# Optimization experiments

Measured on AMD Instinct MI355X. Metric: run time of the kernel, lower is better.

## Reference

```python
import jax, jax.numpy as jnp
import numpy as np

N_NODES = 50000


def _scatter_softmax(alpha, row, n):
    # per-row-segment softmax over edges
    amax = jax.ops.segment_max(alpha, row, num_segments=n)
    amax = jnp.where(jnp.isfinite(amax), amax, 0.0)
    ex = jnp.exp(alpha - amax[row])
    den = jax.ops.segment_sum(ex, row, num_segments=n)
    return ex / den[row]


def setup_inputs() -> dict:
    key = jax.random.key(0)
    ks = jax.random.split(key, 10)
    N, E, H, NC, D = N_NODES, 500000, 128, 3, 3
    kv_in = H + NC * NC  # 137 (edges_in_d = 0)
    h = jax.random.normal(ks[0], (N, H), jnp.float32)
    coord = jax.random.normal(ks[1], (N, NC, D), jnp.float32)
    row = jax.random.randint(ks[2], (E,), 0, N, jnp.int32)
    col = jax.random.randint(ks[3], (E,), 0, N, jnp.int32)
    Wq = jax.random.normal(ks[4], (H, H), jnp.float32) / np.sqrt(H)
    bq = jnp.zeros((H,), jnp.float32)
    Wkv = jax.random.normal(ks[5], (kv_in, 2 * H), jnp.float32) / np.sqrt(kv_in)
    bkv = jnp.zeros((2 * H,), jnp.float32)
    Wc1 = jax.random.normal(ks[6], (H, 4 * H), jnp.float32) / np.sqrt(H)
    # torch.nn.init.xavier_uniform_(..., gain=0.001)
    Wc2 = jax.random.normal(ks[7], (4 * H, NC), jnp.float32) * 0.001
    return {"h": h, "coord": coord, "row": row, "col": col,
            "Wq": Wq, "bq": bq, "Wkv": Wkv, "bkv": bkv, "Wc1": Wc1, "Wc2": Wc2}


def reference(h, coord, row, col, Wq, bq, Wkv, bkv, Wc1, Wc2):
    N = h.shape[0]
    nc = coord.shape[1]
    # coord2radial (rm_F_norm=True: no normalization)
    coord_diff = coord[row] - coord[col]                      # [E, nc, d]
    radial = jnp.einsum('ecd,efd->ecf', coord_diff, coord_diff)  # [E, nc, nc]
    radial_flat = radial.reshape(radial.shape[0], nc * nc)
    # att_model: gather -> Q / KV linears -> interleaved k,v split
    q = h[row] @ Wq + bq                                      # [E, H]
    target_feat = jnp.concatenate([radial_flat, h[col]], axis=1)
    kv = target_feat @ Wkv + bkv                              # [E, 2H]
    k, v = kv[:, 0::2], kv[:, 1::2]
    alpha = jnp.sum(q * k, axis=1)                            # [E]
    alpha = _scatter_softmax(alpha, row, N)
    # node_model: scatter_sum aggregate (dropout is identity at eval)
    agg = jax.ops.segment_sum(alpha[:, None] * v, row, num_segments=N)
    h_out = h + agg
    # coord_model: coord_mlp(v) (MLPwoBias: linear -> SiLU -> linear, no biases)
    coord_v = alpha[:, None] * (jax.nn.silu(v @ Wc1) @ Wc2)   # [E, nc]
    trans = coord_diff * coord_v[:, :, None]                  # [E, nc, d]
    cagg = jax.ops.segment_sum(trans, row, num_segments=N)
    coord_out = coord + jnp.clip(cagg, -10.0, 10.0)
    return (h_out, coord_out, alpha)
```

## Files before the change

### kernel.cpp

```cpp
#include <hip/hip_runtime.h>

#define H 128
#define KV 256
#define CPAD 16

typedef short bf16x8 __attribute__((ext_vector_type(8)));
typedef float f32x4 __attribute__((ext_vector_type(4)));
union FragU { uint4 u; bf16x8 s; };

#define LOG2E 1.44269504088896f
#define LN2   0.69314718055995f

__device__ __forceinline__ float bf2f(unsigned short u) {
  return __uint_as_float(((unsigned)u) << 16);
}
__device__ __forceinline__ unsigned short f2bf(float f) {
  unsigned b = __float_as_uint(f);
  b += 0x7FFFu + ((b >> 16) & 1u);
  return (unsigned short)(b >> 16);
}
__device__ __forceinline__ float fsilu(float x) {
  return x * __builtin_amdgcn_rcpf(1.f + __expf(-x));
}
__device__ __forceinline__ float fexp2(float x) {
  float r;
  asm("v_exp_f32 %0, %1" : "=v"(r) : "v"(x));
  return r;
}
__device__ __forceinline__ float fsilu2(float y) {
  return y * __builtin_amdgcn_rcpf(1.f + fexp2(-y));
}
__device__ __forceinline__ void rad6_from_cd(const float cd[9], float r6[6]) {
  r6[0] = cd[0]*cd[0] + cd[1]*cd[1] + cd[2]*cd[2];
  r6[1] = cd[3]*cd[3] + cd[4]*cd[4] + cd[5]*cd[5];
  r6[2] = cd[6]*cd[6] + cd[7]*cd[7] + cd[8]*cd[8];
  r6[3] = cd[0]*cd[3] + cd[1]*cd[4] + cd[2]*cd[5];
  r6[4] = cd[0]*cd[6] + cd[1]*cd[7] + cd[2]*cd[8];
  r6[5] = cd[3]*cd[6] + cd[4]*cd[7] + cd[5]*cd[8];
}
__constant__ int c_pa[6] = {0,4,8,1,2,5};
__constant__ int c_pb[6] = {0,0,0,3,6,7};

__global__ __launch_bounds__(256) void k_zero(float* __restrict__ p, int n) {
  int i = blockIdx.x * 256 + threadIdx.x;
  if (i < n) p[i] = 0.f;
}
__global__ __launch_bounds__(256) void k_sentinel(float* __restrict__ out, int n) {
  int i = blockIdx.x * 256 + threadIdx.x;
  if (i < n) out[i] = 1000.0f;
}

__global__ __launch_bounds__(256) void k_prep_w1(const float* __restrict__ Wc1,
                                                 uint4* __restrict__ w1f) {
  int t = blockIdx.x*256 + threadIdx.x;
  int g = t >> 6, lane = t & 63;
  int q = g >> 5, kk = (g >> 3) & 3, mt = g & 7;
  int o = q*128 + mt*16 + (lane & 15);
  int kbase = kk*32 + (lane >> 4)*8;
  unsigned s[8];
  #pragma unroll
  for (int j = 0; j < 8; ++j) s[j] = f2bf(Wc1[(kbase+j)*512 + o] * LOG2E);
  uint4 u;
  u.x = s[0] | (s[1]<<16); u.y = s[2] | (s[3]<<16);
  u.z = s[4] | (s[5]<<16); u.w = s[6] | (s[7]<<16);
  w1f[g*64 + lane] = u;
}

__global__ __launch_bounds__(256) void k_prep_wcat(
    const float* __restrict__ Wq, const float* __restrict__ Wkv,
    uint4* __restrict__ wcat_hi, uint4* __restrict__ wcat_lo)
{
  int t = blockIdx.x*256 + threadIdx.x;
  if (t >= 96*64) return;
  int g = t >> 6, lane = t & 63;
  int mt = g & 7, kk = (g >> 3) & 3, q = g >> 5;
  int oo = mt*16 + (lane & 15);
  int kbase = kk*32 + (lane >> 4)*8;
  unsigned shi[8], slo[8];
  #pragma unroll
  for (int j = 0; j < 8; ++j) {
    int k = kbase + j;
    float w;
    if (q == 0)      w = Wq[k*H + oo];
    else if (q == 1) w = Wkv[(9 + k)*KV + 2*oo];
    else             w = Wkv[(9 + k)*KV + 2*oo + 1];
    unsigned hi = f2bf(w);
    float lo = w - bf2f((unsigned short)hi);
    shi[j] = hi; slo[j] = f2bf(lo);
  }
  uint4 uh, ul;
  uh.x = shi[0]|(shi[1]<<16); uh.y = shi[2]|(shi[3]<<16);
  uh.z = shi[4]|(shi[5]<<16); uh.w = shi[6]|(shi[7]<<16);
  ul.x = slo[0]|(slo[1]<<16); ul.y = slo[2]|(slo[3]<<16);
  ul.z = slo[4]|(slo[5]<<16); ul.w = slo[6]|(slo[7]<<16);
  wcat_hi[g*64 + lane] = uh;
  wcat_lo[g*64 + lane] = ul;
}

__global__ __launch_bounds__(256) void k_prep_wr6(const float* __restrict__ Wkv,
                                                  const float* __restrict__ Wc1,
                                                  float* __restrict__ Wr6) {
  int idx = blockIdx.x*256 + threadIdx.x;
  if (idx >= 6*512) return;
  int d = idx >> 9, o = idx & 511;
  float s = 0.f;
  for (int k = 0; k < 128; ++k) {
    float w = Wkv[c_pa[d]*KV + 2*k + 1];
    if (d >= 3) w += Wkv[c_pb[d]*KV + 2*k + 1];
    s += w * Wc1[k*512 + o];
  }
  Wr6[d*512 + o] = s;
}

__global__ __launch_bounds__(256) void k_prep_ar6(
    const float* __restrict__ Wr6, const float* __restrict__ Wc2,
    uint4* __restrict__ ar6f, float* __restrict__ w2p)
{
  int t = threadIdx.x;
  for (int i = t; i < 512; i += 256) {
    int ch = i;
    unsigned b0 = (unsigned)f2bf(Wr6[0*512+ch]*LOG2E) | ((unsigned)f2bf(Wr6[1*512+ch]*LOG2E)<<16);
    unsigned b1 = (unsigned)f2bf(Wr6[2*512+ch]*LOG2E) | ((unsigned)f2bf(Wr6[3*512+ch]*LOG2E)<<16);
    unsigned b2 = (unsigned)f2bf(Wr6[4*512+ch]*LOG2E) | ((unsigned)f2bf(Wr6[5*512+ch]*LOG2E)<<16);
    ar6f[i] = make_uint4(b0, b1, b2, 0u);
  }
  for (int i = t; i < 1536; i += 256) {
    int i4 = i & 3, rest = i >> 2;
    int k = rest % 3, g = rest / 3;
    int ch = (g >> 2)*16 + (g & 3)*4 + i4;
    w2p[i] = Wc2[ch*3 + k] * LN2;
  }
}

__global__ __launch_bounds__(256) void k_hist2(const int* __restrict__ row,
                                               const int* __restrict__ col,
                                               int* __restrict__ cr,
                                               int* __restrict__ cc, int E) {
  int e = blockIdx.x*256 + threadIdx.x;
  if (e >= E) return;
  atomicAdd(&cr[(size_t)row[e]*CPAD], 1);
  atomicAdd(&cc[(size_t)col[e]*CPAD], 1);
}

__global__ __launch_bounds__(1024) void k_scan2(
    const int* __restrict__ cr, int* __restrict__ rstart, int* __restrict__ rcur,
    const int* __restrict__ cc, int* __restrict__ cstart, int* __restrict__ ccur,
    int n) {
  const int* counts = (blockIdx.x == 0) ? cr : cc;
  int* start = (blockIdx.x == 0) ? rstart : cstart;
  int* cursor = (blockIdx.x == 0) ? rcur : ccur;
  __shared__ int wsum[16];
  __shared__ int carry_s;
  const int tid = threadIdx.x, lane = tid & 63, wid = tid >> 6;
  if (tid == 0) carry_s = 0;
  __syncthreads();
  for (int base = 0; base < n; base += 1024) {
    int i = base + tid;
    int v = (i < n) ? counts[(size_t)i*CPAD] : 0;
    int s = v;
    #pragma unroll
    for (int off = 1; off < 64; off <<= 1) {
      int t = __shfl_up(s, off, 64);
      if (lane >= off) s += t;
    }
    if (lane == 63) wsum[wid] = s;
    __syncthreads();
    if (wid == 0 && lane < 16) {
      int w = wsum[lane];
      #pragma unroll
      for (int off = 1; off < 16; off <<= 1) {
        int t = __shfl_up(w, off, 16);
        if (lane >= off) w += t;
      }
      wsum[lane] = w;
    }
    __syncthreads();
    int wexcl = (wid == 0) ? 0 : wsum[wid-1];
    int excl = carry_s + wexcl + (s - v);
    if (i < n) { start[i] = excl; cursor[(size_t)i*CPAD] = excl; }
    __syncthreads();
    if (tid == 0) carry_s += wsum[15];
    __syncthreads();
  }
  if (threadIdx.x == 0) start[n] = carry_s;
}

__global__ __launch_bounds__(256) void k_scatter2(
    const int* __restrict__ row, const int* __restrict__ col,
    int* __restrict__ rcur, int* __restrict__ eidx,
    int* __restrict__ ccur, int* __restrict__ eidx2, int E) {
  int e = blockIdx.x*256 + threadIdx.x;
  if (e >= E) return;
  int pos = atomicAdd(&rcur[(size_t)row[e]*CPAD], 1);
  eidx[pos] = e;
  int pos2 = atomicAdd(&ccur[(size_t)col[e]*CPAD], 1);
  eidx2[pos2] = e;
}

__global__ __launch_bounds__(256) void k_node_mfma(
    const float* __restrict__ h, const uint4* __restrict__ wcat_hi,
    const uint4* __restrict__ wcat_lo, const float* __restrict__ bq,
    const float* __restrict__ bkv, float* __restrict__ qn,
    unsigned short* __restrict__ kn, unsigned short* __restrict__ vn, int N)
{
  __shared__ unsigned vhi[128*64];
  __shared__ unsigned vlo[128*64];
  const int tid = threadIdx.x;
  const int wid = tid >> 6, lane = tid & 63;
  const int quad = lane >> 4, colc = lane & 15;
  const int n0 = blockIdx.x * 128;
  for (int i = 0; i < 32; ++i) {
    int el = i*4 + wid;
    int c = n0 + el; if (c >= N) c = N - 1;
    float2 hv = *((const float2*)(h + (size_t)c*H + 2*lane));
    unsigned h0 = f2bf(hv.x), h1 = f2bf(hv.y);
    float l0 = hv.x - bf2f((unsigned short)h0);
    float l1 = hv.y - bf2f((unsigned short)h1);
    int sw = el*64 + (((lane>>2) ^ (el&15))<<2) + (lane&3);
    vhi[sw] = h0 | (h1<<16);
    vlo[sw] = (unsigned)f2bf(l0) | ((unsigned)f2bf(l1)<<16);
  }
  __syncthreads();
  const int ntbase = wid*32;
  for (int q = 0; q < 3; ++q) {
    f32x4 acc[8][2];
    #pragma unroll
    for (int mt = 0; mt < 8; ++mt)
      #pragma unroll
      for (int nt = 0; nt < 2; ++nt) acc[mt][nt] = (f32x4){0.f,0.f,0.f,0.f};
    #pragma unroll
    for (int kk = 0; kk < 4; ++kk) {
      FragU bhi[2], blo[2];
      #pragma unroll
      for (int nt = 0; nt < 2; ++nt) {
        int rrow = ntbase + nt*16 + colc;
        int ad = rrow*64 + (((kk*4 + quad) ^ (rrow&15))<<2);
        bhi[nt].u = *((const uint4*)&vhi[ad]);
        blo[nt].u = *((const uint4*)&vlo[ad]);
      }
      #pragma unroll
      for (int mt = 0; mt < 8; ++mt) {
        FragU ahi, alo;
        int gidx = (((q*4+kk)*8+mt)<<6) + lane;
        ahi.u = wcat_hi[gidx];
        alo.u = wcat_lo[gidx];
        #pragma unroll
        for (int nt = 0; nt < 2; ++nt) {
          acc[mt][nt] = __builtin_amdgcn_mfma_f32_16x16x32_bf16(
              ahi.s, bhi[nt].s, acc[mt][nt], 0, 0, 0);
          acc[mt][nt] = __builtin_amdgcn_mfma_f32_16x16x32_bf16(
              ahi.s, blo[nt].s, acc[mt][nt], 0, 0, 0);
          acc[mt][nt] = __builtin_amdgcn_mfma_f32_16x16x32_bf16(
              alo.s, bhi[nt].s, acc[mt][nt], 0, 0, 0);
        }
      }
    }
    #pragma unroll
    for (int mt = 0; mt < 8; ++mt)
      #pragma unroll
      for (int nt = 0; nt < 2; ++nt) {
        int node = n0 + ntbase + nt*16 + colc;
        if (node >= N) continue;
        int chq = mt*16 + quad*4;
        if (q == 0) {
          float4 b = *((const float4*)(bq + chq));
          float4 o;
          o.x = acc[mt][nt][0] + b.x; o.y = acc[mt][nt][1] + b.y;
          o.z = acc[mt][nt][2] + b.z; o.w = acc[mt][nt][3] + b.w;
          *((float4*)(qn + (size_t)node*H + chq)) = o;
        } else if (q == 1) {
          unsigned s0 = f2bf(acc[mt][nt][0] + bkv[2*(chq+0)]);
          unsigned s1 = f2bf(acc[mt][nt][1] + bkv[2*(chq+1)]);
          unsigned s2 = f2bf(acc[mt][nt][2] + bkv[2*(chq+2)]);
          unsigned s3 = f2bf(acc[mt][nt][3] + bkv[2*(chq+3)]);
          *((uint2*)(kn + (size_t)node*H + chq)) =
              make_uint2(s0 | (s1<<16), s2 | (s3<<16));
        } else {
          unsigned s0 = f2bf(acc[mt][nt][0] + bkv[2*(chq+0)+1]);
          unsigned s1 = f2bf(acc[mt][nt][1] + bkv[2*(chq+1)+1]);
          unsigned s2 = f2bf(acc[mt][nt][2] + bkv[2*(chq+2)+1]);
          unsigned s3 = f2bf(acc[mt][nt][3] + bkv[2*(chq+3)+1]);
          *((uint2*)(vn + (size_t)node*H + chq)) =
              make_uint2(s0 | (s1<<16), s2 | (s3<<16));
        }
      }
  }
}

__global__ __launch_bounds__(256) void k_qw(
    const float* __restrict__ qn, const float* __restrict__ Wkv,
    float* __restrict__ qwn, int N)
{
  __shared__ float wke6[6*128];
  const int tid = threadIdx.x;
  for (int idx = tid; idx < 6*128; idx += 256) {
    int d = idx >> 7, j = idx & 127;
    float we = Wkv[c_pa[d]*KV + 2*j];
    if (d >= 3) we += Wkv[c_pb[d]*KV + 2*j];
    wke6[idx] = we;
  }
  __syncthreads();
  const int wid = tid >> 6, lane = tid & 63;
  const int n = blockIdx.x*4 + wid;
  if (n >= N) return;
  float q0 = qn[(size_t)n*H + lane];
  float q1 = qn[(size_t)n*H + 64 + lane];
  #pragma unroll
  for (int d = 0; d < 6; ++d) {
    float p = q0*wke6[d*128 + lane] + q1*wke6[d*128 + 64 + lane];
    #pragma unroll
    for (int m = 32; m > 0; m >>= 1) p += __shfl_xor(p, m, 64);
    if (lane == 0) qwn[(size_t)n*6 + d] = p;
  }
}

__global__ __launch_bounds__(256) void k_edge_alpha(
    const float* __restrict__ coord, const int* __restrict__ row,
    const int* __restrict__ col, const int* __restrict__ eidx,
    const float* __restrict__ qn, const unsigned short* __restrict__ knb,
    const float* __restrict__ qwn, float* __restrict__ aout, int E)
{
  int j = blockIdx.x*256 + threadIdx.x;
  if (j >= E) return;
  int e = eidx[j];
  int r = row[e], c = col[e];
  const float4* qp = (const float4*)(qn + (size_t)r*H);
  const uint4* kp = (const uint4*)(knb + (size_t)c*H);
  float d0 = 0.f, d1 = 0.f, d2 = 0.f, d3 = 0.f;
  #pragma unroll 4
  for (int i = 0; i < 16; ++i) {
    uint4 kv = kp[i];
    float4 q0 = qp[2*i], q1 = qp[2*i+1];
    d0 += q0.x*__uint_as_float(kv.x << 16) + q0.y*__uint_as_float(kv.x & 0xffff0000u);
    d1 += q0.z*__uint_as_float(kv.y << 16) + q0.w*__uint_as_float(kv.y & 0xffff0000u);
    d2 += q1.x*__uint_as_float(kv.z << 16) + q1.y*__uint_as_float(kv.z & 0xffff0000u);
    d3 += q1.z*__uint_as_float(kv.w << 16) + q1.w*__uint_as_float(kv.w & 0xffff0000u);
  }
  float cd[9], r6[6];
  #pragma unroll
  for (int i = 0; i < 9; ++i)
    cd[i] = coord[(size_t)r*9 + i] - coord[(size_t)c*9 + i];
  rad6_from_cd(cd, r6);
  float ar = (d0 + d1) + (d2 + d3);
  #pragma unroll
  for (int d = 0; d < 6; ++d) ar += r6[d]*qwn[(size_t)r*6 + d];
  aout[e] = ar;
}

__global__ __launch_bounds__(256) void k_row_soft(
    const float* __restrict__ h, const float* __restrict__ coord,
    const int* __restrict__ col, const float* __restrict__ Wkv,
    const int* __restrict__ row_start, const int* __restrict__ eidx,
    const unsigned* __restrict__ vnu, float* __restrict__ aout,
    float* __restrict__ hout, int N)
{
  __shared__ float wvo6[6*128];
  __shared__ float ws[4][64];
  __shared__ int   cs[4][64];
  const int tid = threadIdx.x;
  for (int idx = tid; idx < 6*128; idx += 256) {
    int d = idx >> 7, jj = idx & 127;
    float wo = Wkv[c_pa[d]*KV + 2*jj + 1];
    if (d >= 3) wo += Wkv[c_pb[d]*KV + 2*jj + 1];
    wvo6[idx] = wo;
  }
  __syncthreads();
  const int wid = tid >> 6, lane = tid & 63;
  const int r = blockIdx.x*4 + wid;
  if (r >= N) return;
  const int js = row_start[r], je = row_start[r+1];
  const int deg = je - js;
  float crd[9];
  #pragma unroll
  for (int i = 0; i < 9; ++i) crd[i] = coord[(size_t)r*9 + i];

  float t6s[6];
  float mn, invl;
  const bool big = (deg > 64);
  if (!big) {
    int e = 0, c = 0;
    float ar = -1e30f;
    float r6[6] = {0.f,0.f,0.f,0.f,0.f,0.f};
    if (lane < deg) {
      e = eidx[js + lane];
      ar = aout[e];
      c = col[e];
      float cd[9];
      #pragma unroll
      for (int i = 0; i < 9; ++i) cd[i] = crd[i] - coord[(size_t)c*9 + i];
      rad6_from_cd(cd, r6);
    }
    float mx = ar;
    #pragma unroll
    for (int m = 32; m > 0; m >>= 1) mx = fmaxf(mx, __shfl_xor(mx, m, 64));
    mn = mx;
    float w = (lane < deg) ? __expf(ar - mn) : 0.f;
    float lw = w;
    #pragma unroll
    for (int m = 32; m > 0; m >>= 1) lw += __shfl_xor(lw, m, 64);
    invl = (deg > 0) ? 1.f/lw : 0.f;
    #pragma unroll
    for (int d = 0; d < 6; ++d) {
      float v = w*r6[d];
      #pragma unroll
      for (int m = 32; m > 0; m >>= 1) v += __shfl_xor(v, m, 64);
      t6s[d] = v;
    }
    ws[wid][lane] = w;
    cs[wid][lane] = c;
    if (lane < deg) aout[e] = w*invl;
  } else {
    float mx = -1e30f;
    for (int j2 = js + lane; j2 < je; j2 += 64)
      mx = fmaxf(mx, aout[eidx[j2]]);
    #pragma unroll
    for (int m = 32; m > 0; m >>= 1) mx = fmaxf(mx, __shfl_xor(mx, m, 64));
    mn = mx;
    float lp = 0.f;
    float t6p[6] = {0.f,0.f,0.f,0.f,0.f,0.f};
    for (int j2 = js + lane; j2 < je; j2 += 64) {
      int e = eidx[j2];
      float ar = aout[e];
      float w = __expf(ar - mn);
      lp += w;
      int c = col[e];
      float cd[9], r6[6];
      #pragma unroll
      for (int i = 0; i < 9; ++i) cd[i] = crd[i] - coord[(size_t)c*9 + i];
      rad6_from_cd(cd, r6);
      #pragma unroll
      for (int d = 0; d < 6; ++d) t6p[d] += w*r6[d];
    }
    #pragma unroll
    for (int m = 32; m > 0; m >>= 1) lp += __shfl_xor(lp, m, 64);
    invl = (deg > 0) ? 1.f/lp : 0.f;
    #pragma unroll
    for (int d = 0; d < 6; ++d) {
      float v = t6p[d];
      #pragma unroll
      for (int m = 32; m > 0; m >>= 1) v += __shfl_xor(v, m, 64);
      t6s[d] = v;
    }
  }
  float acc0 = 0.f, acc1 = 0.f;
  if (!big) {
    #pragma unroll 4
    for (int t = 0; t < deg; ++t) {
      float w = ws[wid][t];
      int c = cs[wid][t];
      unsigned v = vnu[(size_t)c*64 + lane];
      acc0 += w*__uint_as_float(v << 16);
      acc1 += w*__uint_as_float(v & 0xffff0000u);
    }
  } else {
    for (int t = js; t < je; ++t) {
      int e = eidx[t];
      float ar = aout[e];
      float w = __expf(ar - mn);
      int c = col[e];
      unsigned v = vnu[(size_t)c*64 + lane];
      acc0 += w*__uint_as_float(v << 16);
      acc1 += w*__uint_as_float(v & 0xffff0000u);
    }
    for (int j2 = js + lane; j2 < je; j2 += 64) {
      int e = eidx[j2];
      aout[e] = __expf(aout[e] - mn)*invl;
    }
  }
  float o0 = acc0, o1 = acc1;
  #pragma unroll
  for (int d = 0; d < 6; ++d) {
    o0 += t6s[d]*wvo6[d*128 + 2*lane];
    o1 += t6s[d]*wvo6[d*128 + 2*lane + 1];
  }
  hout[(size_t)r*H + 2*lane]     = h[(size_t)r*H + 2*lane]     + o0*invl;
  hout[(size_t)r*H + 2*lane + 1] = h[(size_t)r*H + 2*lane + 1] + o1*invl;
}

__global__ __launch_bounds__(256) void k_node_hn(
    const unsigned* __restrict__ vnu, const uint4* __restrict__ w1f,
    unsigned short* __restrict__ hn, int N)
{
  __shared__ unsigned vt[128*64];
  __shared__ unsigned short hno[128*128];
  const int tid = threadIdx.x;
  const int wid = tid >> 6, lane = tid & 63;
  const int quad = lane >> 4, colc = lane & 15;
  const int n0 = blockIdx.x * 128;
  for (int i = 0; i < 32; ++i) {
    int el = i*4 + wid;
    int c = n0 + el; if (c >= N) c = N - 1;
    unsigned pk = vnu[(size_t)c*64 + lane];
    vt[el*64 + (((lane>>2) ^ (el&15))<<2) + (lane&3)] = pk;
  }
  __syncthreads();
  const int ntbase = wid*32;
  for (int q = 0; q < 4; ++q) {
    f32x4 acc[8][2];
    #pragma unroll
    for (int mt = 0; mt < 8; ++mt)
      #pragma unroll
      for (int nt = 0; nt < 2; ++nt) acc[mt][nt] = (f32x4){0.f,0.f,0.f,0.f};
    #pragma unroll
    for (int kk = 0; kk < 4; ++kk) {
      FragU bfr[2];
      #pragma unroll
      for (int nt = 0; nt < 2; ++nt) {
        int rrow = ntbase + nt*16 + colc;
        int chunk = kk*4 + quad;
        bfr[nt].u = *((const uint4*)&vt[rrow*64 + ((chunk ^ (rrow&15))<<2)]);
      }
      #pragma unroll
      for (int mt = 0; mt < 8; ++mt) {
        FragU afr;
        afr.u = w1f[(((q*4+kk)*8+mt)<<6) + lane];
        #pragma unroll
        for (int nt = 0; nt < 2; ++nt)
          acc[mt][nt] = __builtin_amdgcn_mfma_f32_16x16x32_bf16(
              afr.s, bfr[nt].s, acc[mt][nt], 0, 0, 0);
      }
    }
    #pragma unroll
    for (int mt = 0; mt < 8; ++mt)
      #pragma unroll
      for (int nt = 0; nt < 2; ++nt) {
        int node = ntbase + nt*16 + colc;
        int o = mt*16 + quad*4;
        unsigned lo = (unsigned)f2bf(acc[mt][nt][0]) | ((unsigned)f2bf(acc[mt][nt][1]) << 16);
        unsigned hi = (unsigned)f2bf(acc[mt][nt][2]) | ((unsigned)f2bf(acc[mt][nt][3]) << 16);
        *((uint2*)&hno[node*128 + o]) = make_uint2(lo, hi);
      }
    __syncthreads();
    const uint4* hns = (const uint4*)hno;
    #pragma unroll
    for (int it = 0; it < 8; ++it) {
      int u = it*256 + tid;
      int node = u >> 4, within = u & 15;
      int gn = n0 + node;
      if (gn < N) ((uint4*)hn)[(size_t)gn*64 + q*16 + within] = hns[node*16 + within];
    }
    __syncthreads();
  }
}

__global__ __launch_bounds__(512) void k_edge_mlp3(
    const float* __restrict__ coord, const int* __restrict__ row,
    const int* __restrict__ col, const uint4* __restrict__ ar6f,
    const float* __restrict__ w2p, const unsigned short* __restrict__ hn,
    const int* __restrict__ eidx2, float* __restrict__ mlpout, int E,
    int tbase, int tend)
{
  __shared__ uint4 a8[512];
  __shared__ float4 w2s[384];
  const int tid = threadIdx.x;
  {
    const uint4* s4 = (const uint4*)w2p;
    for (int i = tid; i < 512; i += 512) a8[i] = ar6f[i];
    if (tid < 384) w2s[tid] = ((const float4*)s4)[tid];
  }
  __syncthreads();
  const int wid = tid >> 6, lane = tid & 63;
  const int l15 = lane & 15, quad = lane >> 4;
  const bool q0 = (quad == 0);

  int gw = blockIdx.x*8 + wid;
  int nw = gridDim.x*8;
  for (int t = tbase + gw; t < tend; t += nw) {
    int j = t*64 + lane;
    int jc = (j < E) ? j : (E - 1);
    int e = eidx2[jc];
    int c = col[e];
    int r = row[e];
    float cd[9], r6[6];
    #pragma unroll
    for (int i = 0; i < 9; ++i)
      cd[i] = coord[(size_t)r*9 + i] - coord[(size_t)c*9 + i];
    rad6_from_cd(cd, r6);
    unsigned pw0 = (unsigned)f2bf(r6[0]) | ((unsigned)f2bf(r6[1]) << 16);
    unsigned pw1 = (unsigned)f2bf(r6[2]) | ((unsigned)f2bf(r6[3]) << 16);
    unsigned pw2 = (unsigned)f2bf(r6[4]) | ((unsigned)f2bf(r6[5]) << 16);
    FragU bfr[4];
    const unsigned short* hb[4];
    #pragma unroll
    for (int f = 0; f < 4; ++f) {
      int src = f*16 + l15;
      unsigned w0 = __shfl(pw0, src, 64);
      unsigned w1 = __shfl(pw1, src, 64);
      unsigned w2_ = __shfl(pw2, src, 64);
      bfr[f].u = make_uint4(q0 ? w0 : 0u, q0 ? w1 : 0u, q0 ? w2_ : 0u, 0u);
      int nb = __shfl(c, src, 64);
      hb[f] = hn + (size_t)nb*512 + quad*4;
    }
    float cv[4][3];
    #pragma unroll
    for (int f = 0; f < 4; ++f) { cv[f][0]=0.f; cv[f][1]=0.f; cv[f][2]=0.f; }

    #pragma unroll 2
    for (int m = 0; m < 32; ++m) {
      uint4 av = a8[m*16 + l15];
      FragU afr;
      afr.u = make_uint4(q0 ? av.x : 0u, q0 ? av.y : 0u, q0 ? av.z : 0u, 0u);
      float4 wk0 = w2s[(m*4 + quad)*3 + 0];
      float4 wk1 = w2s[(m*4 + quad)*3 + 1];
      float4 wk2 = w2s[(m*4 + quad)*3 + 2];
      #pragma unroll
      for (int f = 0; f < 4; ++f) {
        uint2 hv = *((const uint2*)(hb[f] + m*16));
        f32x4 cin;
        cin[0] = __uint_as_float(hv.x << 16);
        cin[1] = __uint_as_float(hv.x & 0xffff0000u);
        cin[2] = __uint_as_float(hv.y << 16);
        cin[3] = __uint_as_float(hv.y & 0xffff0000u);
        f32x4 d = __builtin_amdgcn_mfma_f32_16x16x32_bf16(
            afr.s, bfr[f].s, cin, 0, 0, 0);
        float s0 = fsilu2(d[0]);
        float s1 = fsilu2(d[1]);
        float s2 = fsilu2(d[2]);
        float s3 = fsilu2(d[3]);
        cv[f][0] += s0*wk0.x + s1*wk0.y + s2*wk0.z + s3*wk0.w;
        cv[f][1] += s0*wk1.x + s1*wk1.y + s2*wk1.z + s3*wk1.w;
        cv[f][2] += s0*wk2.x + s1*wk2.y + s2*wk2.z + s3*wk2.w;
      }
    }
    #pragma unroll
    for (int f = 0; f < 4; ++f)
      #pragma unroll
      for (int k = 0; k < 3; ++k) {
        float v = cv[f][k];
        v += __shfl_xor(v, 16, 64);
        v += __shfl_xor(v, 32, 64);
        cv[f][k] = v;
      }
    #pragma unroll
    for (int f = 0; f < 4; ++f) {
      int src = f*16 + l15;
      int eb = __shfl(e, src, 64);
      int jb = t*64 + src;
      if (q0 && jb < E) {
        float* mp = &mlpout[(size_t)eb*3];
        mp[0] = cv[f][0]; mp[1] = cv[f][1]; mp[2] = cv[f][2];
      }
    }
  }
}

__global__ __launch_bounds__(256) void k_coord(
    const float* __restrict__ coord, const int* __restrict__ col,
    const int* __restrict__ row_start, const int* __restrict__ eidx,
    const float* __restrict__ aout, const float* __restrict__ mlpout,
    float* __restrict__ cout, int N)
{
  const int tid = threadIdx.x;
  const int wid = tid >> 6, lane = tid & 63;
  const int sub = lane >> 4, sl = lane & 15;
  const int r = blockIdx.x*16 + wid*4 + sub;
  if (r >= N) return;
  const int js = row_start[r], je = row_start[r+1];
  const int deg = je - js;
  float cr[9];
  #pragma unroll
  for (int i = 0; i < 9; ++i) cr[i] = coord[(size_t)r*9 + i];
  float cg[9] = {0.f,0.f,0.f,0.f,0.f,0.f,0.f,0.f,0.f};
  if (deg <= 16) {
    if (sl < deg) {
      int e = eidx[js + sl];
      float a = aout[e];
      int c = col[e];
      float p0 = a*mlpout[(size_t)e*3+0];
      float p1 = a*mlpout[(size_t)e*3+1];
      float p2 = a*mlpout[(size_t)e*3+2];
      #pragma unroll
      for (int d = 0; d < 3; ++d) {
        float c0 = cr[0+d] - coord[(size_t)c*9 + 0+d];
        float c1 = cr[3+d] - coord[(size_t)c*9 + 3+d];
        float c2 = cr[6+d] - coord[(size_t)c*9 + 6+d];
        cg[0+d] = p0*c0; cg[3+d] = p1*c1; cg[6+d] = p2*c2;
      }
    }
  } else {
    for (int j = js + sl; j < je; j += 16) {
      int e = eidx[j];
      float a = aout[e];
      int c = col[e];
      float p0 = a*mlpout[(size_t)e*3+0];
      float p1 = a*mlpout[(size_t)e*3+1];
      float p2 = a*mlpout[(size_t)e*3+2];
      #pragma unroll
      for (int d = 0; d < 3; ++d) {
        cg[0+d] += p0*(cr[0+d] - coord[(size_t)c*9 + 0+d]);
        cg[3+d] += p1*(cr[3+d] - coord[(size_t)c*9 + 3+d]);
        cg[6+d] += p2*(cr[6+d] - coord[(size_t)c*9 + 6+d]);
      }
    }
  }
  #pragma unroll
  for (int i = 0; i < 9; ++i)
    #pragma unroll
    for (int m = 8; m > 0; m >>= 1) cg[i] += __shfl_xor(cg[i], m, 16);
  if (sl == 0) {
    #pragma unroll
    for (int i = 0; i < 9; ++i) {
      float x = fminf(10.f, fmaxf(-10.f, cg[i]));
      cout[(size_t)r*9 + i] = cr[i] + x;
    }
  }
}

extern "C" void kernel_launch(void* const* d_in, const int* in_sizes, int n_in,
                              void* d_out, int out_size, void* d_ws, size_t ws_size,
                              hipStream_t stream)
{
  const float* h     = (const float*)d_in[0];
  const float* coord = (const float*)d_in[1];
  const int* row = (const int*)d_in[2];
  const int* col = (const int*)d_in[3];
  const float* Wq  = (const float*)d_in[4];
  const float* bq  = (const float*)d_in[5];
  const float* Wkv = (const float*)d_in[6];
  const float* bkv = (const float*)d_in[7];
  const float* Wc1 = (const float*)d_in[8];
  const float* Wc2 = (const float*)d_in[9];
  const int N = in_sizes[0] / H;
  const int E = in_sizes[2];
  float* out = (float*)d_out;

  char* p = (char*)d_ws;
  float* qn = (float*)p;
  unsigned short* kn = (unsigned short*)(p + (size_t)N*H*4);
  unsigned short* hn = (unsigned short*)p;
  p += (size_t)N*H*8;
  unsigned short* vn = (unsigned short*)p;  p += (size_t)N*H*2;
  float* mlpout = (float*)p;                p += (size_t)E*3*4;
  int* counts_r = (int*)p;                  p += (size_t)N*CPAD*4;
  int* counts_c = (int*)p;                  p += (size_t)N*CPAD*4;
  int* cursor_r = (int*)p;                  p += (size_t)N*CPAD*4;
  int* cursor_c = (int*)p;                  p += (size_t)N*CPAD*4;
  int* row_start = (int*)p;                 p += (size_t)(N+1)*4;
  int* cstart = (int*)p;                    p += (size_t)(N+1)*4;
  int* eidx = (int*)p;                      p += (size_t)E*4;
  int* eidx2 = (int*)p;                     p += (size_t)E*4;
  uint4* w1f = (uint4*)((((size_t)p) + 15) & ~(size_t)15);
  float* Wr6 = (float*)((char*)w1f + 8192*16);
  uint4* ar6f = (uint4*)((char*)Wr6 + 6*512*4);
  float* w2p  = (float*)((char*)ar6f + 512*16);
  float* qwn  = (float*)((char*)w2p + 1536*4);
  uint4* wcat_hi = (uint4*)((char*)qwn + (size_t)N*6*4);
  uint4* wcat_lo = (uint4*)((char*)wcat_hi + 6144*16);
  const size_t need = (size_t)((char*)wcat_lo + 6144*16 - (char*)d_ws);

  if (ws_size < need) {
    k_sentinel<<<(out_size + 255)/256, 256, 0, stream>>>(out, out_size);
    return;
  }

  float* hout = out;
  float* cout = out + (size_t)N*H;
  float* aout = cout + (size_t)N*9;

  k_zero<<<(2*N*CPAD + 255)/256, 256, 0, stream>>>((float*)counts_r, 2*N*CPAD);
  k_prep_w1<<<32, 256, 0, stream>>>(Wc1, w1f);
  k_prep_wcat<<<24, 256, 0, stream>>>(Wq, Wkv, wcat_hi, wcat_lo);
  k_prep_wr6<<<12, 256, 0, stream>>>(Wkv, Wc1, Wr6);
  k_prep_ar6<<<1, 256, 0, stream>>>(Wr6, Wc2, ar6f, w2p);
  k_hist2<<<(E + 255)/256, 256, 0, stream>>>(row, col, counts_r, counts_c, E);
  k_node_mfma<<<(N + 127)/128, 256, 0, stream>>>(h, wcat_hi, wcat_lo, bq, bkv,
                                                 qn, kn, vn, N);
  k_qw<<<(N + 3)/4, 256, 0, stream>>>(qn, Wkv, qwn, N);
  k_scan2<<<2, 1024, 0, stream>>>(counts_r, row_start, cursor_r,
                                  counts_c, cstart, cursor_c, N);
  k_scatter2<<<(E + 255)/256, 256, 0, stream>>>(row, col, cursor_r, eidx,
                                                cursor_c, eidx2, E);
  k_edge_alpha<<<(E + 255)/256, 256, 0, stream>>>(coord, row, col, eidx,
                                                  qn, kn, qwn, aout, E);
  k_row_soft<<<(N + 3)/4, 256, 0, stream>>>(h, coord, col, Wkv, row_start, eidx,
                                            (const unsigned*)vn, aout, hout, N);
  k_node_hn<<<(N + 127)/128, 256, 0, stream>>>((const unsigned*)vn, w1f, hn, N);
  {
    int ntile = (E + 63) >> 6;
    int half = ntile >> 1;
    k_edge_mlp3<<<512, 512, 0, stream>>>(coord, row, col, ar6f, w2p,
                                         hn, eidx2, mlpout, E, 0, half);
    k_edge_mlp3<<<512, 512, 0, stream>>>(coord, row, col, ar6f, w2p,
                                         hn, eidx2, mlpout, E, half, ntile);
  }
  k_coord<<<(N + 15)/16, 256, 0, stream>>>(coord, col, row_start, eidx, aout,
                                           mlpout, cout, N);
}
```

Measured before the change: 690.0 us.

## Replace two-block serial prefix scan with parallel three-pass scan

The old scan ran one 1024-thread block per array, looping serially over 50000 counts with several barriers per chunk. The new version splits this into three kernels: a block-local scan over 1024-element chunks across many blocks, a single small kernel that scans the per-block sums, and an add pass that applies the block offsets and writes the cursors. This spreads the work over many CUs, at the cost of two extra kernel launches and an extra round trip through global memory for the start array.

```diff
diff --git a/kernel.cpp b/kernel.cpp
--- a/kernel.cpp
+++ b/kernel.cpp
@@ -142,47 +142,81 @@
   atomicAdd(&cc[(size_t)col[e]*CPAD], 1);
 }
 
-__global__ __launch_bounds__(1024) void k_scan2(
-    const int* __restrict__ cr, int* __restrict__ rstart, int* __restrict__ rcur,
-    const int* __restrict__ cc, int* __restrict__ cstart, int* __restrict__ ccur,
-    int n) {
-  const int* counts = (blockIdx.x == 0) ? cr : cc;
-  int* start = (blockIdx.x == 0) ? rstart : cstart;
-  int* cursor = (blockIdx.x == 0) ? rcur : ccur;
-  __shared__ int wsum[16];
-  __shared__ int carry_s;
+__global__ __launch_bounds__(256) void k_scan_local(
+    const int* __restrict__ cr, const int* __restrict__ cc,
+    int* __restrict__ rstart, int* __restrict__ cstart,
+    int* __restrict__ bsum, int n, int nb)
+{
+  int arr = blockIdx.x / nb;
+  int b = blockIdx.x - arr*nb;
+  const int* counts = arr ? cc : cr;
+  int* start = arr ? cstart : rstart;
+  __shared__ int wsum[4];
   const int tid = threadIdx.x, lane = tid & 63, wid = tid >> 6;
-  if (tid == 0) carry_s = 0;
+  int i0 = b*1024 + tid*4;
+  int v0 = (i0+0 < n) ? counts[(size_t)(i0+0)*CPAD] : 0;
+  int v1 = (i0+1 < n) ? counts[(size_t)(i0+1)*CPAD] : 0;
+  int v2 = (i0+2 < n) ? counts[(size_t)(i0+2)*CPAD] : 0;
+  int v3 = (i0+3 < n) ? counts[(size_t)(i0+3)*CPAD] : 0;
+  int t = v0 + v1 + v2 + v3;
+  int s = t;
+  #pragma unroll
+  for (int off = 1; off < 64; off <<= 1) {
+    int u = __shfl_up(s, off, 64);
+    if (lane >= off) s += u;
+  }
+  if (lane == 63) wsum[wid] = s;
   __syncthreads();
-  for (int base = 0; base < n; base += 1024) {
-    int i = base + tid;
-    int v = (i < n) ? counts[(size_t)i*CPAD] : 0;
+  int wexcl = 0;
+  #pragma unroll
+  for (int w = 0; w < 3; ++w) if (wid > w) wexcl += wsum[w];
+  int texcl = wexcl + (s - t);
+  if (i0+0 < n) start[i0+0] = texcl;
+  if (i0+1 < n) start[i0+1] = texcl + v0;
+  if (i0+2 < n) start[i0+2] = texcl + v0 + v1;
+  if (i0+3 < n) start[i0+3] = texcl + v0 + v1 + v2;
+  if (tid == 255) bsum[blockIdx.x] = wexcl + s;
+}
+
+__global__ __launch_bounds__(128) void k_scan_mid(
+    const int* __restrict__ bsum, int* __restrict__ boff,
+    int* __restrict__ rstart, int* __restrict__ cstart, int n, int nb)
+{
+  int arr = threadIdx.x >> 6, lane = threadIdx.x & 63;
+  int carry = 0;
+  for (int base = 0; base < nb; base += 64) {
+    int i = base + lane;
+    int v = (i < nb) ? bsum[arr*nb + i] : 0;
     int s = v;
     #pragma unroll
     for (int off = 1; off < 64; off <<= 1) {
-      int t = __shfl_up(s, off, 64);
-      if (lane >= off) s += t;
-    }
-    if (lane == 63) wsum[wid] = s;
-    __syncthreads();
-    if (wid == 0 && lane < 16) {
-      int w = wsum[lane];
-      #pragma unroll
-      for (int off = 1; off < 16; off <<= 1) {
-        int t = __shfl_up(w, off, 16);
-        if (lane >= off) w += t;
-      }
-      wsum[lane] = w;
-    }
-    __syncthreads();
-    int wexcl = (wid == 0) ? 0 : wsum[wid-1];
-    int excl = carry_s + wexcl + (s - v);
-    if (i < n) { start[i] = excl; cursor[(size_t)i*CPAD] = excl; }
-    __syncthreads();
-    if (tid == 0) carry_s += wsum[15];
-    __syncthreads();
-  }
-  if (threadIdx.x == 0) start[n] = carry_s;
+      int u = __shfl_up(s, off, 64);
+      if (lane >= off) s += u;
+    }
+    if (i < nb) boff[arr*nb + i] = carry + s - v;
+    carry += __shfl(s, 63, 64);
+  }
+  if (lane == 0) {
+    if (arr == 0) rstart[n] = carry; else cstart[n] = carry;
+  }
+}
+
+__global__ __launch_bounds__(256) void k_scan_add(
+    int* __restrict__ rstart, int* __restrict__ rcur,
+    int* __restrict__ cstart, int* __restrict__ ccur,
+    const int* __restrict__ boff, int n, int nb)
+{
+  int idx = blockIdx.x*256 + threadIdx.x;
+  if (idx >= 2*n) return;
+  int arr = (idx >= n) ? 1 : 0;
+  int i = arr ? (idx - n) : idx;
+  int b = i >> 10;
+  int off = boff[arr*nb + b];
+  int* start = arr ? cstart : rstart;
+  int* cur = arr ? ccur : rcur;
+  int sv = start[i] + off;
+  start[i] = sv;
+  cur[(size_t)i*CPAD] = sv;
 }
 
 __global__ __launch_bounds__(256) void k_scatter2(
@@ -739,6 +773,8 @@
   int* cstart = (int*)p;                    p += (size_t)(N+1)*4;
   int* eidx = (int*)p;                      p += (size_t)E*4;
   int* eidx2 = (int*)p;                     p += (size_t)E*4;
+  int* bsum = (int*)p;                      p += (size_t)2048*4;
+  int* boff = (int*)p;                      p += (size_t)2048*4;
   uint4* w1f = (uint4*)((((size_t)p) + 15) & ~(size_t)15);
   float* Wr6 = (float*)((char*)w1f + 8192*16);
   uint4* ar6f = (uint4*)((char*)Wr6 + 6*512*4);
@@ -756,6 +792,8 @@
   float* hout = out;
   float* cout = out + (size_t)N*H;
   float* aout = cout + (size_t)N*9;
+
+  const int nb = (N + 1023) >> 10;
 
   k_zero<<<(2*N*CPAD + 255)/256, 256, 0, stream>>>((float*)counts_r, 2*N*CPAD);
   k_prep_w1<<<32, 256, 0, stream>>>(Wc1, w1f);
@@ -766,8 +804,11 @@
   k_node_mfma<<<(N + 127)/128, 256, 0, stream>>>(h, wcat_hi, wcat_lo, bq, bkv,
                                                  qn, kn, vn, N);
   k_qw<<<(N + 3)/4, 256, 0, stream>>>(qn, Wkv, qwn, N);
-  k_scan2<<<2, 1024, 0, stream>>>(counts_r, row_start, cursor_r,
-                                  counts_c, cstart, cursor_c, N);
+  k_scan_local<<<2*nb, 256, 0, stream>>>(counts_r, counts_c, row_start, cstart,
+                                         bsum, N, nb);
+  k_scan_mid<<<1, 128, 0, stream>>>(bsum, boff, row_start, cstart, N, nb);
+  k_scan_add<<<(2*N + 255)/256, 256, 0, stream>>>(row_start, cursor_r,
+                                                  cstart, cursor_c, boff, N, nb);
   k_scatter2<<<(E + 255)/256, 256, 0, stream>>>(row, col, cursor_r, eidx,
                                                 cursor_c, eidx2, E);
   k_edge_alpha<<<(E + 255)/256, 256, 0, stream>>>(coord, row, col, eidx,
```

Result: faster. 614.0 us (-11.0%).
